# Performance work log

Hardware: AMD Instinct MI355X
Metric: run time of the kernel (lower is better)

## Reference

```python
import jax, jax.numpy as jnp
import numpy as np

B, T, H, W, C = 2, 3, 128, 128, 128
HEADS, D = 8, 16
CK = HEADS * D
RY, RX = 2, 2
PH, PW = 2 * RY + 1, 2 * RX + 1
S = PH * PW  # 25 spatial offsets


def setup_inputs() -> dict:
    key = jax.random.key(0)
    ks = jax.random.split(key, 7)
    std = 0.05
    return {
        "values": jax.random.normal(ks[0], (B, T, H, W, C), jnp.float32),
        "Wq": jax.random.normal(ks[1], (C, CK), jnp.float32) * std,
        "Wk": jax.random.normal(ks[2], (C, CK), jnp.float32) * std,
        "Wv": jax.random.normal(ks[3], (C, CK), jnp.float32) * std,
        "Wo": jax.random.normal(ks[4], (CK, C), jnp.float32) * std,
        "temp_emb": jax.random.normal(ks[5], (T, C), jnp.float32) * std,
        "spatial_emb": jax.random.normal(ks[6], (S, CK), jnp.float32) * std,
    }


def reference(values, Wq, Wk, Wv, Wo, temp_emb, spatial_emb):
    # values: [B,T,H,W,C].  Intra mode, training path: queries = all T frames.
    # add temporal embedding to keys (and queries, since intra non-inference
    # gathers all frames: Q input == K input)
    kin = values + temp_emb[None, :, None, None, :]                 # [B,T,H,W,C]
    K_all = jnp.einsum('bthwc,ck->bthwk', kin, Wk)                  # [B,T,H,W,Ck]
    V_all = jnp.einsum('bthwc,ck->bthwk', values, Wv)               # [B,T,H,W,Ck]

    # clipped patch centers (border pixels reuse the nearest interior patch)
    y = jnp.arange(H); cy = jnp.clip(y, RY, H - RY - 1)
    x = jnp.arange(W); cx = jnp.clip(x, RX, W - RX - 1)
    # per-query relative position inside its patch -> query spatial embedding
    q_sp_idx = (y - cy + RY)[:, None] * PW + (x - cx + RX)[None, :]  # [H,W]
    q_sp_emb = spatial_emb[q_sp_idx]                                 # [H,W,Ck]

    Q = jnp.einsum('bthwc,ck->bthwk', kin, Wq) + q_sp_emb            # [B,Q,H,W,Ck]
    Qh = Q.reshape(B, T, H, W, HEADS, D)

    # spatial offsets, dy outer / dx inner => offset s == spatial emb row s
    dys = jnp.repeat(jnp.arange(-RY, RY + 1), PW)                    # [S]
    dxs = jnp.tile(jnp.arange(-RX, RX + 1), PH)                      # [S]
    ny_all = jnp.clip(cy[None, :] + dys[:, None], 0, H - 1)          # [S,H]
    nx_all = jnp.clip(cx[None, :] + dxs[:, None], 0, W - 1)          # [S,W]

    scale = jax.lax.rsqrt(jnp.float32(D))

    def score_step(_, inp):
        ny, nx, emb = inp                                            # [H],[W],[Ck]
        K_n = K_all[:, :, ny][:, :, :, nx] + emb                     # [B,T,H,W,Ck]
        K_nh = K_n.reshape(B, T, H, W, HEADS, D)
        s = jnp.einsum('bqhwnd,bthwnd->bqthwn', Qh, K_nh) * scale    # [B,Q,T,H,W,n]
        return None, s

    _, scores = jax.lax.scan(score_step, None, (ny_all, nx_all, spatial_emb))
    # [S,B,Q,T,H,W,n] -> [B,Q,H,W,n,S,T]
    scores = jnp.transpose(scores, (1, 2, 4, 5, 6, 0, 3))
    w = jax.nn.softmax(scores.reshape(B, T, H, W, HEADS, S * T), axis=-1)
    w = w.reshape(B, T, H, W, HEADS, S, T)

    w_s_first = jnp.moveaxis(w, 5, 0)                                # [S,B,Q,H,W,n,T]

    def out_step(acc, inp):
        ny, nx, w_s = inp                                            # w_s: [B,Q,H,W,n,T]
        V_n = V_all[:, :, ny][:, :, :, nx].reshape(B, T, H, W, HEADS, D)
        return acc + jnp.einsum('bqhwnt,bthwnd->bqhwnd', w_s, V_n), None

    out0 = jnp.zeros((B, T, H, W, HEADS, D), Qh.dtype)
    out, _ = jax.lax.scan(out_step, out0, (ny_all, nx_all, w_s_first))
    out = out.reshape(B, T, H, W, CK)
    return jnp.einsum('bqhwk,kc->bqhwc', out, Wo)                    # [B,Q,H,W,C]
```

## Files before the change

### kernel.cpp

```cpp
#include <hip/hip_runtime.h>
#include <hip/hip_fp16.h>
#include <math.h>

constexpr int B_ = 2, T_ = 3, H_ = 128, W_ = 128, C_ = 128;
constexpr int HEADS_ = 8, D_ = 16, CK_ = 128;
constexpr int RY_ = 2, RX_ = 2, PH_ = 5, PW_ = 5, S_ = 25;
constexpr int NTOK = B_ * T_ * H_ * W_;

typedef float     f32x4 __attribute__((ext_vector_type(4)));
typedef _Float16  f16x2 __attribute__((ext_vector_type(2)));
typedef _Float16  f16x4 __attribute__((ext_vector_type(4)));
typedef _Float16  f16x8 __attribute__((ext_vector_type(8)));

static __device__ __forceinline__ f32x4 mfma16(f16x4 a, f16x4 b, f32x4 c) {
#if __has_builtin(__builtin_amdgcn_mfma_f32_16x16x16f16)
  return __builtin_amdgcn_mfma_f32_16x16x16f16(a, b, c, 0, 0, 0);
#else
  asm volatile("v_mfma_f32_16x16x16_f16 %0, %1, %2, %0" : "+v"(c) : "v"(a), "v"(b));
  return c;
#endif
}

union U32H2 { unsigned u; f16x2 h; __half2 hh; };

static __device__ __forceinline__ f16x2 pkrtz(float a, float b) {
  return __builtin_bit_cast(f16x2, __builtin_amdgcn_cvt_pkrtz(a, b));
}

static __device__ __forceinline__ unsigned pk_exp2(f16x2 x) {
  U32H2 in, out;
  in.h = x;
  out.hh = h2exp2(in.hh);
  return out.u;
}

__global__ __launch_bounds__(256) void prep(
    const float* __restrict__ Wq, const float* __restrict__ Wk,
    const float* __restrict__ Wv, const float* __restrict__ Wo,
    const float* __restrict__ sp, const float* __restrict__ te,
    _Float16* __restrict__ WT, _Float16* __restrict__ WoT,
    _Float16* __restrict__ spH, float* __restrict__ tv)
{
  const int idx = blockIdx.x * 256 + threadIdx.x;
  if (idx < 49152) {
    const int m = idx >> 14, j = idx & 16383, n = j >> 7, k = j & 127;
    const float* Wm = (m == 0) ? Wq : ((m == 1) ? Wk : Wv);
    WT[idx] = (_Float16)Wm[k * 128 + n];
  } else if (idx < 65536) {
    const int j = idx - 49152, n = j >> 7, k = j & 127;
    WoT[j] = (_Float16)Wo[k * 128 + n];
  } else if (idx < 69632) {
    const int j = idx - 65536, s = j >> 7, c = j & 127;
    spH[j] = (s < 25) ? (_Float16)sp[s * 128 + c] : (_Float16)0.f;
  } else if (idx < 70016) {
    const int j = idx - 69632, t = j >> 7, n = j & 127;
    float a = 0.f;
    for (int c = 0; c < 128; ++c) a += te[t * 128 + c] * Wv[c * 128 + n];
    tv[j] = a;
  }
}

__global__ __launch_bounds__(256, 3) void qkv_mfma(
    const float* __restrict__ values, const _Float16* __restrict__ WT,
    const float* __restrict__ temp_emb, const float* __restrict__ spatial_emb,
    const float* __restrict__ tv,
    _Float16* __restrict__ Qh, _Float16* __restrict__ Kh, _Float16* __restrict__ Vh)
{
  __shared__ __align__(16) _Float16 kin_s[64][140];
  const int tid = threadIdx.x;
  const int tok0 = blockIdx.x * 64;
  const int t = (tok0 >> 14) % T_;

  for (int i = tid; i < 64 * 32; i += 256) {
    const int tk = i >> 5, cg = i & 31;
    const float4 v = *(const float4*)&values[(size_t)(tok0 + tk) * C_ + cg * 4];
    const float4 e = *(const float4*)&temp_emb[t * C_ + cg * 4];
    f16x4 kv;
    kv[0] = (_Float16)(v.x + e.x); kv[1] = (_Float16)(v.y + e.y);
    kv[2] = (_Float16)(v.z + e.z); kv[3] = (_Float16)(v.w + e.w);
    *(f16x4*)&kin_s[tk][cg * 4] = kv;
  }

  const int l = tid & 63, w = tid >> 6, l15 = l & 15, g = l >> 4;
  const _Float16* Wbase = WT + (size_t)(w * 96) * 128;

  f16x4 acur[6], anxt[6];
#pragma unroll
  for (int j = 0; j < 6; ++j)
    acur[j] = *(const f16x4*)&Wbase[(size_t)(j * 16 + l15) * 128 + 4 * g];

  __syncthreads();

  f32x4 acc[6][4];
#pragma unroll
  for (int j = 0; j < 6; ++j)
#pragma unroll
    for (int tt = 0; tt < 4; ++tt) acc[j][tt] = (f32x4){0.f, 0.f, 0.f, 0.f};

#pragma unroll
  for (int kc = 0; kc < 8; ++kc) {
    if (kc < 7) {
      const int kon = (kc + 1) * 16 + 4 * g;
#pragma unroll
      for (int j = 0; j < 6; ++j)
        anxt[j] = *(const f16x4*)&Wbase[(size_t)(j * 16 + l15) * 128 + kon];
    }
    const int ko = kc * 16 + 4 * g;
    f16x4 bfr[4];
#pragma unroll
    for (int tt = 0; tt < 4; ++tt)
      bfr[tt] = *(const f16x4*)&kin_s[tt * 16 + l15][ko];
#pragma unroll
    for (int j = 0; j < 6; ++j)
#pragma unroll
      for (int tt = 0; tt < 4; ++tt)
        acc[j][tt] = mfma16(acur[j], bfr[tt], acc[j][tt]);
#pragma unroll
    for (int j = 0; j < 6; ++j) acur[j] = anxt[j];
  }

  constexpr float CSC = 0.25f * 1.44269504088896f;
#pragma unroll
  for (int j = 0; j < 6; ++j) {
    const int ntile = w * 6 + j;
    const int ch0 = (ntile & 7) * 16 + 4 * g;
#pragma unroll
    for (int tt = 0; tt < 4; ++tt) {
      const int tok = tok0 + tt * 16 + l15;
      const size_t o = (size_t)tok * CK_ + ch0;
      f16x4 r;
      if (ntile < 8) {
        const int x = tok & 127, y = (tok >> 7) & 127;
        const int cy = min(max(y, RY_), H_ - 1 - RY_);
        const int cx = min(max(x, RX_), W_ - 1 - RX_);
        const int qsp = (y - cy + RY_) * PW_ + (x - cx + RX_);
        const float4 e = *(const float4*)&spatial_emb[qsp * CK_ + ch0];
        r[0] = (_Float16)((acc[j][tt][0] + e.x) * CSC);
        r[1] = (_Float16)((acc[j][tt][1] + e.y) * CSC);
        r[2] = (_Float16)((acc[j][tt][2] + e.z) * CSC);
        r[3] = (_Float16)((acc[j][tt][3] + e.w) * CSC);
        *(f16x4*)&Qh[o] = r;
      } else if (ntile < 16) {
        r[0] = (_Float16)acc[j][tt][0]; r[1] = (_Float16)acc[j][tt][1];
        r[2] = (_Float16)acc[j][tt][2]; r[3] = (_Float16)acc[j][tt][3];
        *(f16x4*)&Kh[o] = r;
      } else {
        const float4 tve = *(const float4*)&tv[t * 128 + ch0];
        r[0] = (_Float16)(acc[j][tt][0] - tve.x);
        r[1] = (_Float16)(acc[j][tt][1] - tve.y);
        r[2] = (_Float16)(acc[j][tt][2] - tve.z);
        r[3] = (_Float16)(acc[j][tt][3] - tve.w);
        *(f16x4*)&Vh[o] = r;
      }
    }
  }
}

__global__ __launch_bounds__(256) void attn_mfma(
    const _Float16* __restrict__ Q, const _Float16* __restrict__ K,
    const _Float16* __restrict__ V, const _Float16* __restrict__ spH,
    _Float16* __restrict__ ck)
{
  __shared__ __align__(16) _Float16 K_s[192 * 40];
  __shared__ __align__(16) _Float16 V_s[192 * 44];
  __shared__ __align__(8)  _Float16 qe_s[2 * 64 * 26];
  __shared__ float l_s[4][2][16];

  const int tid = threadIdx.x;
  const int bid0 = blockIdx.x;
  const int bid = (bid0 & 7) * 768 + (bid0 >> 3);
  const int hq = bid & 3;
  const int tile = bid >> 2;
  const int tx = tile & 15, ty = (tile >> 4) & 15, img = tile >> 8;
  const int b = img / 3;
  const int y0 = ty * 8, x0 = tx * 8;
  const int rowbase = max(y0, 2) - 2;
  const int colbase = max(x0, 2) - 2;
  const int tokbase = img * 16384 + y0 * 128 + x0;
  const int chb = hq * 32;

  const int l = tid & 63, wv = tid >> 6, l15 = l & 15, g = l >> 4;
  const int q_glob = wv * 16 + l15;
  const int qy = 2 * wv + (l15 >> 3), qx = l15 & 7;
  const int y = y0 + qy, x = x0 + qx;
  const int tok = tokbase + qy * 128 + qx;
  const int cy = min(max(y, 2), 125), cx = min(max(x, 2), 125);
  const int myryc = cy - rowbase;
  const int rxc = cx - colbase;
  const int dxpbase = 4 * g - rxc + 2;

  const int rycA = min(max(y0 + 2 * wv,     2), 125) - rowbase;
  const int rycB = min(max(y0 + 2 * wv + 1, 2), 125) - rowbase;
  const int rymin = min(min(rycA, rycB) - 2, 6);

  bool vx[4];
#pragma unroll
  for (int i = 0; i < 4; ++i) vx[i] = (unsigned)(dxpbase + i) <= 4u;

  int poff[6], ldoffK[6], ldoffV[6];
#pragma unroll
  for (int it = 0; it < 6; ++it) {
    const int idx = tid + it * 256;
    const int row = idx >> 3, cg = idx & 7;
    const int ny = min(rowbase + (row >> 4), 127);
    const int nx = min(colbase + (row & 15), 127);
    poff[it] = (ny * 128 + nx) * CK_ + chb + cg * 4;
    ldoffK[it] = row * 40 + cg * 4;
    ldoffV[it] = row * 44 + cg * 4;
  }
  const size_t imgstep = (size_t)16384 * CK_;
  const _Float16* Kp = K + (size_t)(b * 3) * imgstep;
  const _Float16* Vp = V + (size_t)(b * 3) * imgstep;

  f16x4 kpre[6], vpre[6];
#pragma unroll
  for (int it = 0; it < 6; ++it) {
    kpre[it] = *(const f16x4*)&Kp[poff[it]];
    vpre[it] = *(const f16x4*)&Vp[poff[it]];
  }

  f16x4 qfrag[2];
#pragma unroll
  for (int h = 0; h < 2; ++h)
    qfrag[h] = *(const f16x4*)&Q[(size_t)tok * CK_ + chb + h * 16 + 4 * g];

#pragma unroll
  for (int h = 0; h < 2; ++h) {
    const int qrow = (h * 64 + q_glob) * 26;
#pragma unroll
    for (int mt = 0; mt < 2; ++mt) {
      const f16x4 a = *(const f16x4*)&spH[(size_t)(mt * 16 + l15) * 128 + chb + h * 16 + 4 * g];
      f32x4 c = {0.f, 0.f, 0.f, 0.f};
      c = mfma16(a, qfrag[h], c);
      const int s0w = mt * 16 + 4 * g;
      if (mt == 0 || g < 2) {
        U32H2 p01, p23;
        p01.h = pkrtz(c[0], c[1]);
        p23.h = pkrtz(c[2], c[3]);
        *(unsigned*)&qe_s[qrow + s0w]     = p01.u;
        *(unsigned*)&qe_s[qrow + s0w + 2] = p23.u;
      } else if (g == 2) {
        qe_s[qrow + 24] = (_Float16)c[0];
      }
    }
  }
  if (g == 0) {
    qe_s[(0 * 64 + q_glob) * 26 + 25] = (_Float16)(-30000.0f);
    qe_s[(1 * 64 + q_glob) * 26 + 25] = (_Float16)(-30000.0f);
  }

  f32x4 o_acc[2];
  float l_acc[2];
#pragma unroll
  for (int h = 0; h < 2; ++h) { o_acc[h] = (f32x4){0.f, 0.f, 0.f, 0.f}; l_acc[h] = 0.f; }

  const f16x2 ones2 = {(_Float16)1.f, (_Float16)1.f};

#pragma unroll
  for (int t = 0; t < 3; ++t) {
    if (t) __syncthreads();
#pragma unroll
    for (int it = 0; it < 6; ++it) {
      *(f16x4*)&K_s[ldoffK[it]] = kpre[it];
      *(f16x4*)&V_s[ldoffV[it]] = vpre[it];
    }
    __syncthreads();
    if (t < 2) {
      const _Float16* Kt = Kp + (size_t)(t + 1) * imgstep;
      const _Float16* Vt = Vp + (size_t)(t + 1) * imgstep;
#pragma unroll
      for (int it = 0; it < 6; ++it) {
        kpre[it] = *(const f16x4*)&Kt[poff[it]];
        vpre[it] = *(const f16x4*)&Vt[poff[it]];
      }
    }

    __builtin_amdgcn_s_setprio(1);
    f16x4 wfr[2][6];
#pragma unroll
    for (int jj = 0; jj < 6; ++jj) {
      const int nt = rymin + jj;
      f32x4 c0 = {0.f, 0.f, 0.f, 0.f}, c1 = {0.f, 0.f, 0.f, 0.f};
      {
        const f16x4 a0 = *(const f16x4*)&K_s[(nt * 16 + l15) * 40 + 4 * g];
        const f16x4 a1 = *(const f16x4*)&K_s[(nt * 16 + l15) * 40 + 16 + 4 * g];
        c0 = mfma16(a0, qfrag[0], c0);
        c1 = mfma16(a1, qfrag[1], c1);
      }
      const int dyp = nt - myryc + 2;
      const bool vy = (unsigned)dyp <= 4u;
      const int s0 = dyp * 5 + dxpbase;
      int si[4];
#pragma unroll
      for (int i = 0; i < 4; ++i) si[i] = (vy && vx[i]) ? s0 + i : 25;
#pragma unroll
      for (int h = 0; h < 2; ++h) {
        const f32x4 c = h ? c1 : c0;
        const int qb = (h * 64 + q_glob) * 26;
        U32H2 q01, q23;
        q01.u = (unsigned)(unsigned short)__builtin_bit_cast(short, qe_s[qb + si[0]])
              | ((unsigned)(unsigned short)__builtin_bit_cast(short, qe_s[qb + si[1]]) << 16);
        q23.u = (unsigned)(unsigned short)__builtin_bit_cast(short, qe_s[qb + si[2]])
              | ((unsigned)(unsigned short)__builtin_bit_cast(short, qe_s[qb + si[3]]) << 16);
        const f16x2 s01 = pkrtz(c[0], c[1]) + q01.h;
        const f16x2 s23 = pkrtz(c[2], c[3]) + q23.h;
        U32H2 p01, p23;
        p01.u = pk_exp2(s01);
        p23.u = pk_exp2(s23);
        l_acc[h] = __builtin_amdgcn_fdot2(p01.h, ones2, l_acc[h], false);
        l_acc[h] = __builtin_amdgcn_fdot2(p23.h, ones2, l_acc[h], false);
        union { unsigned u[2]; f16x4 v; } wu;
        wu.u[0] = p01.u; wu.u[1] = p23.u;
        wfr[h][jj] = wu.v;
      }
    }

#pragma unroll
    for (int h = 0; h < 2; ++h) {
#pragma unroll
      for (int jj = 0; jj < 6; ++jj) {
        const int nt = rymin + jj;
        f16x4 bv;
#pragma unroll
        for (int i = 0; i < 4; ++i)
          bv[i] = V_s[(nt * 16 + 4 * g + i) * 44 + h * 16 + l15];
        o_acc[h] = mfma16(wfr[h][jj], bv, o_acc[h]);
      }
    }
    __builtin_amdgcn_s_setprio(0);
  }

#pragma unroll
  for (int h = 0; h < 2; ++h) {
    float lt = l_acc[h];
    lt += __shfl_xor(lt, 16);
    lt += __shfl_xor(lt, 32);
    if (l < 16) l_s[wv][h][l15] = 1.f / lt;
  }
#pragma unroll
  for (int h = 0; h < 2; ++h) {
#pragma unroll
    for (int i = 0; i < 4; ++i) {
      const int q = 4 * g + i;
      const float inv = l_s[wv][h][q];
      const int qtok = tokbase + (2 * wv + (q >> 3)) * 128 + (q & 7);
      ck[(size_t)qtok * CK_ + chb + h * 16 + l15] = (_Float16)(o_acc[h][i] * inv);
    }
  }
}

__global__ __launch_bounds__(256) void out_mfma(
    const _Float16* __restrict__ ck, const _Float16* __restrict__ WoT,
    float* __restrict__ out)
{
  __shared__ __align__(16) _Float16 ck_s[128][152];
  const int tid = threadIdx.x;
  const int tok0 = blockIdx.x * 128;

  for (int i = tid; i < 128 * 16; i += 256) {
    const int tk = i >> 4, cg = i & 15;
    *(f16x8*)&ck_s[tk][cg * 8] = *(const f16x8*)&ck[(size_t)(tok0 + tk) * C_ + cg * 8];
  }
  __syncthreads();

  const int l = tid & 63, w = tid >> 6, l15 = l & 15, g = l >> 4;

  f32x4 acc[2][8];
#pragma unroll
  for (int j = 0; j < 2; ++j)
#pragma unroll
    for (int tt = 0; tt < 8; ++tt) acc[j][tt] = (f32x4){0.f, 0.f, 0.f, 0.f};

  for (int kc = 0; kc < 8; ++kc) {
    const int ko = kc * 16 + 4 * g;
    f16x4 bfr[8];
#pragma unroll
    for (int tt = 0; tt < 8; ++tt)
      bfr[tt] = *(const f16x4*)&ck_s[tt * 16 + l15][ko];
#pragma unroll
    for (int j = 0; j < 2; ++j) {
      const f16x4 a = *(const f16x4*)&WoT[(size_t)((w * 2 + j) * 16 + l15) * 128 + ko];
#pragma unroll
      for (int tt = 0; tt < 8; ++tt)
        acc[j][tt] = mfma16(a, bfr[tt], acc[j][tt]);
    }
  }

#pragma unroll
  for (int j = 0; j < 2; ++j) {
    const int ch0 = (w * 2 + j) * 16 + 4 * g;
#pragma unroll
    for (int tt = 0; tt < 8; ++tt) {
      const int tok = tok0 + tt * 16 + l15;
      float4 ov;
      ov.x = acc[j][tt][0]; ov.y = acc[j][tt][1];
      ov.z = acc[j][tt][2]; ov.w = acc[j][tt][3];
      *(float4*)&out[(size_t)tok * C_ + ch0] = ov;
    }
  }
}

extern "C" void kernel_launch(void* const* d_in, const int* in_sizes, int n_in,
                              void* d_out, int out_size, void* d_ws, size_t ws_size,
                              hipStream_t stream) {
    const float* values      = (const float*)d_in[0];
    const float* Wq          = (const float*)d_in[1];
    const float* Wk          = (const float*)d_in[2];
    const float* Wv          = (const float*)d_in[3];
    const float* Wo          = (const float*)d_in[4];
    const float* temp_emb    = (const float*)d_in[5];
    const float* spatial_emb = (const float*)d_in[6];
    float* out = (float*)d_out;

    const size_t NC = (size_t)NTOK * CK_;
    _Float16* Qh  = (_Float16*)d_ws;
    _Float16* Kh  = Qh  + NC;
    _Float16* Vh  = Kh  + NC;
    _Float16* ckh = Vh  + NC;
    _Float16* WT  = ckh + NC;
    _Float16* WoT = WT  + 49152;
    _Float16* spH = WoT + 16384;
    float*    tv  = (float*)(spH + 4096);

    prep<<<274, 256, 0, stream>>>(Wq, Wk, Wv, Wo, spatial_emb, temp_emb,
                                  WT, WoT, spH, tv);
    qkv_mfma<<<NTOK / 64, 256, 0, stream>>>(values, WT, temp_emb, spatial_emb,
                                            tv, Qh, Kh, Vh);
    attn_mfma<<<6144, 256, 0, stream>>>(Qh, Kh, Vh, spH, ckh);
    out_mfma<<<NTOK / 128, 256, 0, stream>>>(ckh, WoT, out);
}
```

Measured before the change: 169.6 us.

## Fuse output projection into attention kernel with 1024-thread full-channel blocks

The attention and output-projection kernels are merged. Each block now covers all four head groups of an 8x8 tile with 1024 threads and stages the full 128-channel K/V halo in dynamic shared memory. The normalized attention output is written into shared memory that reuses the K region, and the Wo projection is applied in the same block. This removes the global round trip of the intermediate fp16 ck tensor and one kernel launch. In exchange it needs about 133 KB of LDS per block, so only one block fits per CU, and the launch-bounds hint may restrict registers.

```diff
diff --git a/kernel.cpp b/kernel.cpp
--- a/kernel.cpp
+++ b/kernel.cpp
@@ -33,6 +33,11 @@
   out.hh = h2exp2(in.hh);
   return out.u;
 }
+
+constexpr int KV_STRIDE = 136;
+constexpr int KV_ELEMS  = 192 * KV_STRIDE;
+constexpr int QE_ELEMS  = 8 * 64 * 26;
+constexpr size_t SMEM_BYTES = (size_t)(2 * KV_ELEMS + QE_ELEMS) * 2 + 16 * 2 * 16 * 4;
 
 __global__ __launch_bounds__(256) void prep(
     const float* __restrict__ Wq, const float* __restrict__ Wk,
@@ -156,32 +161,35 @@
   }
 }
 
-__global__ __launch_bounds__(256) void attn_mfma(
+__global__ __launch_bounds__(1024, 4) void attn_fused(
     const _Float16* __restrict__ Q, const _Float16* __restrict__ K,
     const _Float16* __restrict__ V, const _Float16* __restrict__ spH,
-    _Float16* __restrict__ ck)
+    const _Float16* __restrict__ WoT, float* __restrict__ out)
 {
-  __shared__ __align__(16) _Float16 K_s[192 * 40];
-  __shared__ __align__(16) _Float16 V_s[192 * 44];
-  __shared__ __align__(8)  _Float16 qe_s[2 * 64 * 26];
-  __shared__ float l_s[4][2][16];
+  extern __shared__ __align__(16) _Float16 smem[];
+  _Float16* K_s  = smem;
+  _Float16* V_s  = K_s + KV_ELEMS;
+  _Float16* qe_s = V_s + KV_ELEMS;
+  float*    l_s  = (float*)(qe_s + QE_ELEMS);
+  _Float16* ck_s = K_s;
 
   const int tid = threadIdx.x;
   const int bid0 = blockIdx.x;
-  const int bid = (bid0 & 7) * 768 + (bid0 >> 3);
-  const int hq = bid & 3;
-  const int tile = bid >> 2;
+  const int tile = (bid0 & 7) * 192 + (bid0 >> 3);
   const int tx = tile & 15, ty = (tile >> 4) & 15, img = tile >> 8;
   const int b = img / 3;
   const int y0 = ty * 8, x0 = tx * 8;
   const int rowbase = max(y0, 2) - 2;
   const int colbase = max(x0, 2) - 2;
   const int tokbase = img * 16384 + y0 * 128 + x0;
+
+  const int wv5 = tid >> 6;
+  const int hq  = wv5 >> 2;
+  const int wvq = wv5 & 3;
   const int chb = hq * 32;
-
-  const int l = tid & 63, wv = tid >> 6, l15 = l & 15, g = l >> 4;
-  const int q_glob = wv * 16 + l15;
-  const int qy = 2 * wv + (l15 >> 3), qx = l15 & 7;
+  const int l = tid & 63, l15 = l & 15, g = l >> 4;
+  const int q_glob = wvq * 16 + l15;
+  const int qy = 2 * wvq + (l15 >> 3), qx = l15 & 7;
   const int y = y0 + qy, x = x0 + qx;
   const int tok = tokbase + qy * 128 + qx;
   const int cy = min(max(y, 2), 125), cx = min(max(x, 2), 125);
@@ -189,24 +197,23 @@
   const int rxc = cx - colbase;
   const int dxpbase = 4 * g - rxc + 2;
 
-  const int rycA = min(max(y0 + 2 * wv,     2), 125) - rowbase;
-  const int rycB = min(max(y0 + 2 * wv + 1, 2), 125) - rowbase;
+  const int rycA = min(max(y0 + 2 * wvq,     2), 125) - rowbase;
+  const int rycB = min(max(y0 + 2 * wvq + 1, 2), 125) - rowbase;
   const int rymin = min(min(rycA, rycB) - 2, 6);
 
   bool vx[4];
 #pragma unroll
   for (int i = 0; i < 4; ++i) vx[i] = (unsigned)(dxpbase + i) <= 4u;
 
-  int poff[6], ldoffK[6], ldoffV[6];
+  int poff[6], ldoff[6];
 #pragma unroll
   for (int it = 0; it < 6; ++it) {
-    const int idx = tid + it * 256;
-    const int row = idx >> 3, cg = idx & 7;
+    const int idx = tid + it * 1024;
+    const int row = idx >> 5, cg = idx & 31;
     const int ny = min(rowbase + (row >> 4), 127);
     const int nx = min(colbase + (row & 15), 127);
-    poff[it] = (ny * 128 + nx) * CK_ + chb + cg * 4;
-    ldoffK[it] = row * 40 + cg * 4;
-    ldoffV[it] = row * 44 + cg * 4;
+    poff[it] = (ny * 128 + nx) * CK_ + cg * 4;
+    ldoff[it] = row * KV_STRIDE + cg * 4;
   }
   const size_t imgstep = (size_t)16384 * CK_;
   const _Float16* Kp = K + (size_t)(b * 3) * imgstep;
@@ -226,7 +233,7 @@
 
 #pragma unroll
   for (int h = 0; h < 2; ++h) {
-    const int qrow = (h * 64 + q_glob) * 26;
+    const int qrow = ((hq * 2 + h) * 64 + q_glob) * 26;
 #pragma unroll
     for (int mt = 0; mt < 2; ++mt) {
       const f16x4 a = *(const f16x4*)&spH[(size_t)(mt * 16 + l15) * 128 + chb + h * 16 + 4 * g];
@@ -245,8 +252,8 @@
     }
   }
   if (g == 0) {
-    qe_s[(0 * 64 + q_glob) * 26 + 25] = (_Float16)(-30000.0f);
-    qe_s[(1 * 64 + q_glob) * 26 + 25] = (_Float16)(-30000.0f);
+    qe_s[((hq * 2 + 0) * 64 + q_glob) * 26 + 25] = (_Float16)(-30000.0f);
+    qe_s[((hq * 2 + 1) * 64 + q_glob) * 26 + 25] = (_Float16)(-30000.0f);
   }
 
   f32x4 o_acc[2];
@@ -261,8 +268,8 @@
     if (t) __syncthreads();
 #pragma unroll
     for (int it = 0; it < 6; ++it) {
-      *(f16x4*)&K_s[ldoffK[it]] = kpre[it];
-      *(f16x4*)&V_s[ldoffV[it]] = vpre[it];
+      *(f16x4*)&K_s[ldoff[it]] = kpre[it];
+      *(f16x4*)&V_s[ldoff[it]] = vpre[it];
     }
     __syncthreads();
     if (t < 2) {
@@ -282,8 +289,8 @@
       const int nt = rymin + jj;
       f32x4 c0 = {0.f, 0.f, 0.f, 0.f}, c1 = {0.f, 0.f, 0.f, 0.f};
       {
-        const f16x4 a0 = *(const f16x4*)&K_s[(nt * 16 + l15) * 40 + 4 * g];
-        const f16x4 a1 = *(const f16x4*)&K_s[(nt * 16 + l15) * 40 + 16 + 4 * g];
+        const f16x4 a0 = *(const f16x4*)&K_s[(nt * 16 + l15) * KV_STRIDE + chb + 4 * g];
+        const f16x4 a1 = *(const f16x4*)&K_s[(nt * 16 + l15) * KV_STRIDE + chb + 16 + 4 * g];
         c0 = mfma16(a0, qfrag[0], c0);
         c1 = mfma16(a1, qfrag[1], c1);
       }
@@ -296,7 +303,7 @@
 #pragma unroll
       for (int h = 0; h < 2; ++h) {
         const f32x4 c = h ? c1 : c0;
-        const int qb = (h * 64 + q_glob) * 26;
+        const int qb = ((hq * 2 + h) * 64 + q_glob) * 26;
         U32H2 q01, q23;
         q01.u = (unsigned)(unsigned short)__builtin_bit_cast(short, qe_s[qb + si[0]])
               | ((unsigned)(unsigned short)__builtin_bit_cast(short, qe_s[qb + si[1]]) << 16);
@@ -323,7 +330,7 @@
         f16x4 bv;
 #pragma unroll
         for (int i = 0; i < 4; ++i)
-          bv[i] = V_s[(nt * 16 + 4 * g + i) * 44 + h * 16 + l15];
+          bv[i] = V_s[(nt * 16 + 4 * g + i) * KV_STRIDE + chb + h * 16 + l15];
         o_acc[h] = mfma16(wfr[h][jj], bv, o_acc[h]);
       }
     }
@@ -335,68 +342,46 @@
     float lt = l_acc[h];
     lt += __shfl_xor(lt, 16);
     lt += __shfl_xor(lt, 32);
-    if (l < 16) l_s[wv][h][l15] = 1.f / lt;
-  }
+    if (l < 16) l_s[(wv5 * 2 + h) * 16 + l15] = 1.f / lt;
+  }
+  __syncthreads();
+
 #pragma unroll
   for (int h = 0; h < 2; ++h) {
 #pragma unroll
     for (int i = 0; i < 4; ++i) {
       const int q = 4 * g + i;
-      const float inv = l_s[wv][h][q];
-      const int qtok = tokbase + (2 * wv + (q >> 3)) * 128 + (q & 7);
-      ck[(size_t)qtok * CK_ + chb + h * 16 + l15] = (_Float16)(o_acc[h][i] * inv);
-    }
-  }
-}
-
-__global__ __launch_bounds__(256) void out_mfma(
-    const _Float16* __restrict__ ck, const _Float16* __restrict__ WoT,
-    float* __restrict__ out)
-{
-  __shared__ __align__(16) _Float16 ck_s[128][152];
-  const int tid = threadIdx.x;
-  const int tok0 = blockIdx.x * 128;
-
-  for (int i = tid; i < 128 * 16; i += 256) {
-    const int tk = i >> 4, cg = i & 15;
-    *(f16x8*)&ck_s[tk][cg * 8] = *(const f16x8*)&ck[(size_t)(tok0 + tk) * C_ + cg * 8];
+      const float inv = l_s[(wv5 * 2 + h) * 16 + q];
+      const int lt = wvq * 16 + (q >> 3) * 8 + (q & 7);
+      ck_s[lt * KV_STRIDE + chb + h * 16 + l15] = (_Float16)(o_acc[h][i] * inv);
+    }
   }
   __syncthreads();
 
-  const int l = tid & 63, w = tid >> 6, l15 = l & 15, g = l >> 4;
-
-  f32x4 acc[2][8];
-#pragma unroll
-  for (int j = 0; j < 2; ++j)
-#pragma unroll
-    for (int tt = 0; tt < 8; ++tt) acc[j][tt] = (f32x4){0.f, 0.f, 0.f, 0.f};
-
+  const int n  = wv5 >> 1;
+  const int w1 = wv5 & 1;
+  f32x4 acc2[2];
+  acc2[0] = (f32x4){0.f, 0.f, 0.f, 0.f};
+  acc2[1] = (f32x4){0.f, 0.f, 0.f, 0.f};
+#pragma unroll
   for (int kc = 0; kc < 8; ++kc) {
     const int ko = kc * 16 + 4 * g;
-    f16x4 bfr[8];
-#pragma unroll
-    for (int tt = 0; tt < 8; ++tt)
-      bfr[tt] = *(const f16x4*)&ck_s[tt * 16 + l15][ko];
+    const f16x4 a = *(const f16x4*)&WoT[(size_t)(n * 16 + l15) * 128 + ko];
 #pragma unroll
     for (int j = 0; j < 2; ++j) {
-      const f16x4 a = *(const f16x4*)&WoT[(size_t)((w * 2 + j) * 16 + l15) * 128 + ko];
-#pragma unroll
-      for (int tt = 0; tt < 8; ++tt)
-        acc[j][tt] = mfma16(a, bfr[tt], acc[j][tt]);
-    }
-  }
-
+      const int tt = w1 * 2 + j;
+      const f16x4 bc = *(const f16x4*)&ck_s[(tt * 16 + l15) * KV_STRIDE + ko];
+      acc2[j] = mfma16(a, bc, acc2[j]);
+    }
+  }
 #pragma unroll
   for (int j = 0; j < 2; ++j) {
-    const int ch0 = (w * 2 + j) * 16 + 4 * g;
-#pragma unroll
-    for (int tt = 0; tt < 8; ++tt) {
-      const int tok = tok0 + tt * 16 + l15;
-      float4 ov;
-      ov.x = acc[j][tt][0]; ov.y = acc[j][tt][1];
-      ov.z = acc[j][tt][2]; ov.w = acc[j][tt][3];
-      *(float4*)&out[(size_t)tok * C_ + ch0] = ov;
-    }
+    const int tt = w1 * 2 + j;
+    const int lt = tt * 16 + l15;
+    const int gtok = tokbase + (lt >> 3) * 128 + (lt & 7);
+    float4 ov;
+    ov.x = acc2[j][0]; ov.y = acc2[j][1]; ov.z = acc2[j][2]; ov.w = acc2[j][3];
+    *(float4*)&out[(size_t)gtok * C_ + n * 16 + 4 * g] = ov;
   }
 }
 
@@ -416,16 +401,18 @@
     _Float16* Qh  = (_Float16*)d_ws;
     _Float16* Kh  = Qh  + NC;
     _Float16* Vh  = Kh  + NC;
-    _Float16* ckh = Vh  + NC;
-    _Float16* WT  = ckh + NC;
+    _Float16* WT  = Vh  + NC;
     _Float16* WoT = WT  + 49152;
     _Float16* spH = WoT + 16384;
     float*    tv  = (float*)(spH + 4096);
+
+    (void)hipFuncSetAttribute((const void*)attn_fused,
+                              hipFuncAttributeMaxDynamicSharedMemorySize,
+                              (int)SMEM_BYTES);
 
     prep<<<274, 256, 0, stream>>>(Wq, Wk, Wv, Wo, spatial_emb, temp_emb,
                                   WT, WoT, spH, tv);
     qkv_mfma<<<NTOK / 64, 256, 0, stream>>>(values, WT, temp_emb, spatial_emb,
                                             tv, Qh, Kh, Vh);
-    attn_mfma<<<6144, 256, 0, stream>>>(Qh, Kh, Vh, spH, ckh);
-    out_mfma<<<NTOK / 128, 256, 0, stream>>>(ckh, WoT, out);
-}
+    attn_fused<<<1536, 1024, SMEM_BYTES, stream>>>(Qh, Kh, Vh, spH, WoT, out);
+}
```

Measured after the change: 200.4 us. +18.1%, slower.
